# Kernel tuning notes

Measured on AMD Instinct MI355X. Metric: run time of the kernel, lower is better.

Reference implementation:

```python
import jax, jax.numpy as jnp
import numpy as np

B, S, E, H, WIN = 1, 2048, 1024, 16, 256
D = E // H  # head_out = 64


def setup_inputs() -> dict:
    key = jax.random.key(0)
    ks = jax.random.split(key, 10)
    w = lambda k: jax.random.normal(k, (E, E), jnp.float32) * 0.02
    return {
        'x': jax.random.normal(ks[0], (B, S, E), jnp.float32),
        'global_attention_mask': jax.random.randint(ks[1], (B, S), 0, 2).astype(jnp.int32),
        'W_local_query': w(ks[2]),
        'W_local_key': w(ks[3]),
        'W_local_value': w(ks[4]),
        'W_query': w(ks[5]),
        'W_key': w(ks[6]),
        'W_value': w(ks[7]),
        'W_proj': w(ks[8]),
        'b_proj': jnp.zeros((E,), jnp.float32),
    }


def reference(x, global_attention_mask, W_local_query, W_local_key, W_local_value,
              W_query, W_key, W_value, W_proj, b_proj):
    b, seq, emb = x.shape
    nH, dh, win = H, D, WIN
    chunks = seq // win
    NEG = -1e9
    scale = 1.0 / (dh ** 0.5)

    # ---- local (windowed) branch ----
    ql = x @ W_local_query            # [b,S,E]
    kl = x @ W_local_key
    vl = x @ W_local_value
    # NOTE: original does a direct .view -> plain reshape (no head transpose)
    qc = ql.reshape(b, nH, chunks, win, dh)
    kc = kl.reshape(b, nH, chunks, win, dh)
    vloc = vl.reshape(b, nH, seq, dh)
    s = jnp.einsum('bhcqd,bhckd->bhcqk', qc, kc)      # [b,H,C,W,W]
    causal_w = jnp.tril(jnp.ones((win, win), bool))
    s = jnp.where(causal_w, s, NEG) * scale           # mask then /sqrt(d), as in source
    s = s.mean(axis=2)                                # mean over chunks -> [b,H,W,W]
    s = jnp.pad(s, ((0, 0), (0, 0), (0, seq - win), (0, seq - win)))
    aw_l = jax.nn.softmax(s, axis=-1)                 # [b,H,S,S]
    local_ctx = jnp.einsum('bhqk,bhkd->bqhd', aw_l, vloc).reshape(b, seq, emb)

    # ---- global (full) branch ----
    q = (x @ W_query).reshape(b, seq, nH, dh).transpose(0, 2, 1, 3)
    k = (x @ W_key).reshape(b, seq, nH, dh).transpose(0, 2, 1, 3)
    v = (x @ W_value).reshape(b, seq, nH, dh).transpose(0, 2, 1, 3)
    sg = jnp.einsum('bhqd,bhkd->bhqk', q, k)          # [b,H,S,S]
    causal_s = jnp.tril(jnp.ones((seq, seq), bool))
    sg = jnp.where(causal_s, sg, NEG) * scale
    aw_g = jax.nn.softmax(sg, axis=-1)
    gctx = jnp.einsum('bhqk,bhkd->bqhd', aw_g, v).reshape(b, seq, emb)

    # ---- combine via global mask, then output projection ----
    ctx = jnp.where(global_attention_mask[:, :, None] == 1, gctx, local_ctx)
    return ctx @ W_proj + b_proj
```

## Files before the change

### kernel.cpp

```cpp
#include <hip/hip_runtime.h>
#include <hip/hip_bf16.h>

typedef _Float16 h8 __attribute__((ext_vector_type(8)));
typedef _Float16 h4 __attribute__((ext_vector_type(4)));
typedef _Float16 h2 __attribute__((ext_vector_type(2)));
typedef __fp16 fp16x2 __attribute__((ext_vector_type(2)));
typedef float f4 __attribute__((ext_vector_type(4)));

#define S_LEN 2048
#define EMB 1024
#define NH 16
#define DH 64

__device__ __forceinline__ void async_copy16(const void* g, void* l) {
  __builtin_amdgcn_global_load_lds(
      (const __attribute__((address_space(1))) void*)g,
      (__attribute__((address_space(3))) void*)l, 16, 0, 0);
}

__device__ __forceinline__ f4 mfma16(h8 a, h8 b, f4 c) {
  return __builtin_amdgcn_mfma_f32_16x16x32_f16(a, b, c, 0, 0, 0);
}

__device__ __forceinline__ h2 cvt_pk(float a, float b) {
  const fp16x2 r = __builtin_amdgcn_cvt_pkrtz(a, b);
  return __builtin_bit_cast(h2, r);
}

__global__ __launch_bounds__(256) void prep_kernel(
    const float* __restrict__ x, const float* w0, const float* w1, const float* w2,
    const float* w3, const float* w4, const float* w5, const float* w6,
    _Float16* __restrict__ xh, _Float16* __restrict__ Wtb,
    const int* __restrict__ gmask, int* __restrict__ qsel, int* __restrict__ qcnt) {
  const int bid = blockIdx.x;
  if (bid < 2048) {
    const int i = bid * 256 + threadIdx.x;
    const float4 v = *(const float4*)&x[(long)i * 4];
    h4 o;
    o.x = (_Float16)v.x; o.y = (_Float16)v.y; o.z = (_Float16)v.z; o.w = (_Float16)v.w;
    *(h4*)&xh[(long)i * 4] = o;
    return;
  }
  if (bid < 9216) {
    const int b2 = bid - 2048;
    const int z = b2 >> 10, rem = b2 & 1023;
    const float* W = w0;
    switch (z) {
      case 1: W = w1; break; case 2: W = w2; break; case 3: W = w3; break;
      case 4: W = w4; break; case 5: W = w5; break; case 6: W = w6; break;
      default: break;
    }
    __shared__ float t[32][33];
    const int bk = (rem & 31) * 32, bn = (rem >> 5) * 32;
    const int tx = threadIdx.x & 31, ty = threadIdx.x >> 5;
    #pragma unroll
    for (int i = 0; i < 4; ++i)
      t[ty + i * 8][tx] = W[(long)(bk + ty + i * 8) * 1024 + bn + tx];
    __syncthreads();
    _Float16* o = Wtb + (long)z * 1048576;
    #pragma unroll
    for (int i = 0; i < 4; ++i)
      o[(long)(bn + ty + i * 8) * 1024 + bk + tx] = (_Float16)t[tx][ty + i * 8];
    return;
  }
  const int t = threadIdx.x;
  int m8[8], cnt8 = 0;
  #pragma unroll
  for (int j = 0; j < 8; ++j) {
    m8[j] = gmask[t * 8 + j];
    cnt8 += (m8[j] == 1);
  }
  __shared__ int sc[256];
  sc[t] = cnt8;
  __syncthreads();
  for (int off = 1; off < 256; off <<= 1) {
    const int v = (t >= off) ? sc[t - off] : 0;
    __syncthreads();
    sc[t] += v;
    __syncthreads();
  }
  int base = sc[t] - cnt8;
  #pragma unroll
  for (int j = 0; j < 8; ++j)
    if (m8[j] == 1) qsel[base++] = t * 8 + j;
  if (t == 255) qcnt[0] = sc[255];
}

__global__ __launch_bounds__(512, 2) void gemm256_kernel(
    const _Float16* __restrict__ A, const _Float16* __restrict__ Bt,
    _Float16* __restrict__ Aq, _Float16* __restrict__ Ak,
    _Float16* __restrict__ proj234, _Float16* __restrict__ vgT) {
  const int bid = blockIdx.x;
  const int bxx = (bid >> 3) & 7;
  const int byy = (bid & 7) * 3 + (bid >> 6);
  const int bm = bxx * 256, bn = byy * 256;

  __shared__ alignas(16) _Float16 As[2][2][8192];
  __shared__ alignas(16) _Float16 Bs[2][2][8192];

  const int tid = threadIdx.x;
  const int w = tid >> 6, l = tid & 63;
  const int lo = l & 15, hi = l >> 4;
  const int wm = w >> 2, wn = w & 3;
  const int srow = tid >> 3;
  const int kseg = (tid & 7) ^ (srow & 7);

  const _Float16* Bb = Bt + (long)(byy >> 2) * 1048576 + (long)(bn & 1023) * 1024;

#define STG_A(db, half, tt) do {                                                     \
    const int t_ = (tt) < 15 ? (tt) : 15;                                            \
    const _Float16* s_ = A + (long)(bm + (half) * 128 + srow) * 1024 + t_ * 64 + kseg * 8; \
    async_copy16(s_, &As[db][half][w * 512]);                                        \
    async_copy16(s_ + 65536, &As[db][half][4096 + w * 512]);                         \
  } while (0)
#define STG_B(db, half, tt) do {                                                     \
    const int t_ = (tt) < 15 ? (tt) : 15;                                            \
    const _Float16* s_ = Bb + (long)((half) * 128 + srow) * 1024 + t_ * 64 + kseg * 8; \
    async_copy16(s_, &Bs[db][half][w * 512]);                                        \
    async_copy16(s_ + 65536, &Bs[db][half][4096 + w * 512]);                         \
  } while (0)
#define LDA(db, mg) do { _Pragma("unroll")                                           \
    for (int fr = 0; fr < 4; ++fr) {                                                 \
      const int rr = wm * 64 + fr * 16 + lo;                                         \
      _Pragma("unroll") for (int kk = 0; kk < 2; ++kk)                               \
        af[fr][kk] = *(const h8*)&As[db][mg][rr * 64 + (((kk * 4 + hi) ^ (rr & 7)) * 8)]; \
    } } while (0)
#define LDB(db, ng) do { _Pragma("unroll")                                           \
    for (int fc = 0; fc < 2; ++fc) {                                                 \
      const int rr = wn * 32 + fc * 16 + lo;                                         \
      _Pragma("unroll") for (int kk = 0; kk < 2; ++kk)                               \
        bf[ng][fc][kk] = *(const h8*)&Bs[db][ng][rr * 64 + (((kk * 4 + hi) ^ (rr & 7)) * 8)]; \
    } } while (0)
#define MFMA_PH(mg, ng) do {                                                         \
    __builtin_amdgcn_s_setprio(1);                                                   \
    _Pragma("unroll") for (int fr = 0; fr < 4; ++fr)                                 \
      _Pragma("unroll") for (int fc = 0; fc < 2; ++fc) {                             \
        acc[mg][fr][ng][fc] = mfma16(af[fr][0], bf[ng][fc][0], acc[mg][fr][ng][fc]); \
        acc[mg][fr][ng][fc] = mfma16(af[fr][1], bf[ng][fc][1], acc[mg][fr][ng][fc]); \
      }                                                                              \
    __builtin_amdgcn_s_setprio(0);                                                   \
  } while (0)
#define BARR do { asm volatile("" ::: "memory"); __builtin_amdgcn_s_barrier();       \
                  asm volatile("" ::: "memory"); } while (0)
#define VM8 asm volatile("s_waitcnt vmcnt(8)" ::: "memory")

  const f4 zero = {0.f, 0.f, 0.f, 0.f};
  f4 acc[2][4][2][2];
  #pragma unroll
  for (int a_ = 0; a_ < 2; ++a_)
    #pragma unroll
    for (int b_ = 0; b_ < 4; ++b_)
      #pragma unroll
      for (int c_ = 0; c_ < 2; ++c_)
        #pragma unroll
        for (int d_ = 0; d_ < 2; ++d_) acc[a_][b_][c_][d_] = zero;
  h8 af[4][2];
  h8 bf[2][2][2];

  STG_A(0, 0, 0); STG_B(0, 0, 0); STG_A(0, 1, 0); STG_B(0, 1, 0);
  STG_A(1, 0, 1); STG_B(1, 0, 1); STG_A(1, 1, 1);
  asm volatile("s_waitcnt vmcnt(4)" ::: "memory");
  BARR;

  for (int i = 0; i < 8; ++i) {
    const int t2 = 2 * i + 2, t3 = 2 * i + 3;
    LDA(0, 0); LDB(0, 0); STG_B(1, 1, 2 * i + 1); MFMA_PH(0, 0); VM8; BARR;
    LDB(0, 1); STG_A(0, 0, t2); MFMA_PH(0, 1); BARR;
    LDA(0, 1); STG_B(0, 0, t2); MFMA_PH(1, 0); BARR;
    STG_A(0, 1, t2); MFMA_PH(1, 1); VM8; BARR;
    LDA(1, 0); LDB(1, 0); STG_B(0, 1, t2); MFMA_PH(0, 0); VM8; BARR;
    LDB(1, 1); STG_A(1, 0, t3); MFMA_PH(0, 1); BARR;
    LDA(1, 1); STG_B(1, 0, t3); MFMA_PH(1, 0); BARR;
    STG_A(1, 1, t3); MFMA_PH(1, 1); VM8; BARR;
  }

  const int slabv = byy >> 2;
  #pragma unroll
  for (int mg = 0; mg < 2; ++mg)
    #pragma unroll
    for (int fr = 0; fr < 4; ++fr) {
      const int row0 = bm + mg * 128 + wm * 64 + fr * 16 + hi * 4;
      #pragma unroll
      for (int ng = 0; ng < 2; ++ng)
        #pragma unroll
        for (int fc = 0; fc < 2; ++fc) {
          const int colg = bn + ng * 128 + wn * 32 + fc * 16 + lo;
          const int e = colg & 1023;
          if (slabv <= 1) {
            _Float16* dst = (slabv == 0) ? Aq : Ak;
            #pragma unroll
            for (int r = 0; r < 4; ++r) {
              const int s = row0 + r;
              const long off = (long)(((s >> 7) * 256 + (s & 15) * 16 + (e >> 6))) * 512
                               + ((s >> 4) & 7) * 64 + (e & 63);
              dst[off] = (_Float16)acc[mg][fr][ng][fc][r];
            }
          } else if (slabv == 5) {
            const h2 a = cvt_pk(acc[mg][fr][ng][fc][0], acc[mg][fr][ng][fc][1]);
            const h2 b = cvt_pk(acc[mg][fr][ng][fc][2], acc[mg][fr][ng][fc][3]);
            const h4 v4 = {a[0], a[1], b[0], b[1]};
            *(h4*)&vgT[(long)e * 2048 + row0] = v4;
          } else {
            _Float16* cp = proj234 + (long)(slabv - 2) * 2097152 + (long)row0 * 1024 + e;
            #pragma unroll
            for (int r = 0; r < 4; ++r)
              cp[(long)r * 1024] = (_Float16)acc[mg][fr][ng][fc][r];
          }
        }
    }
#undef STG_A
#undef STG_B
#undef LDA
#undef LDB
#undef MFMA_PH
#undef BARR
#undef VM8
}

__global__ __launch_bounds__(256) void flash_kernel(
    const _Float16* __restrict__ Q, const _Float16* __restrict__ Km,
    const _Float16* __restrict__ Vt, const int* __restrict__ qsel,
    const int* __restrict__ qcnt, _Float16* __restrict__ ctx,
    _Float16* __restrict__ pO, float2* __restrict__ ml,
    const _Float16* __restrict__ Aq, const _Float16* __restrict__ Ak,
    _Float16* __restrict__ P, const _Float16* __restrict__ vl,
    float* __restrict__ Vall, float* __restrict__ Vtail) {
  __shared__ alignas(16) char smem[43008];
  const int bx = blockIdx.x;
  const int tid = threadIdx.x;

  if (bx >= 1280) {
    const int hh = bx - 1280;
    const int d = tid & 63, g = tid >> 6;
    float sall = 0.f, shead = 0.f;
    for (int i = 0; i < 32; ++i) {
      const int ro = g * 32 + i;
      const _Float16* base = vl + (long)(hh * 128 + ro) * 1024 + d;
      #pragma unroll
      for (int j = 0; j < 16; ++j) {
        const float v = (float)base[j * 64];
        sall += v;
        if (ro < 16) shead += v;
      }
    }
    float* sA = (float*)smem;
    float* sH = (float*)(smem + 1024);
    sA[g * 64 + d] = sall; sH[g * 64 + d] = shead;
    __syncthreads();
    if (g == 0) {
      const float a = sA[d] + sA[64 + d] + sA[128 + d] + sA[192 + d];
      const float hsum = sH[d] + sH[64 + d] + sH[128 + d] + sH[192 + d];
      Vall[hh * 64 + d] = a;
      Vtail[hh * 64 + d] = a - hsum;
    }
    return;
  }

  if (bx >= 1024) {
    const int b = bx - 1024;
    const int hh = b >> 4, sub = b & 15;
    const int bm = (sub >> 2) * 64, bn = (sub & 3) * 64;
    const _Float16* Ab = Aq + (long)hh * 131072;
    const _Float16* Bb = Ak + (long)hh * 131072;
    _Float16* As = (_Float16*)smem;
    _Float16* Bs = (_Float16*)(smem + 8192);
    const int w = tid >> 6, l = tid & 63;
    const int lo = l & 15, hi = l >> 4;
    const int srow = tid >> 3;
    const int ssl = (tid & 7) ^ (srow & 7);

    const f4 zero = {0.f, 0.f, 0.f, 0.f};
    f4 acc[4];
    #pragma unroll
    for (int n = 0; n < 4; ++n) acc[n] = zero;

    for (int k0 = 0; k0 < 512; k0 += 64) {
      async_copy16(&Ab[(long)(bm + srow) * 512 + k0 + ssl * 8], &As[(w * 8) * 64]);
      async_copy16(&Ab[(long)(bm + 32 + srow) * 512 + k0 + ssl * 8], &As[(w * 8 + 32) * 64]);
      async_copy16(&Bb[(long)(bn + srow) * 512 + k0 + ssl * 8], &Bs[(w * 8) * 64]);
      async_copy16(&Bb[(long)(bn + 32 + srow) * 512 + k0 + ssl * 8], &Bs[(w * 8 + 32) * 64]);
      __syncthreads();
      #pragma unroll
      for (int kk = 0; kk < 2; ++kk) {
        const int ra = w * 16 + lo;
        const h8 af = *(const h8*)&As[ra * 64 + (((kk * 4 + hi) ^ (ra & 7)) * 8)];
        #pragma unroll
        for (int n = 0; n < 4; ++n) {
          const int rb = n * 16 + lo;
          const h8 bff = *(const h8*)&Bs[rb * 64 + (((kk * 4 + hi) ^ (rb & 7)) * 8)];
          acc[n] = mfma16(af, bff, acc[n]);
        }
      }
      __syncthreads();
    }
    #pragma unroll
    for (int n = 0; n < 4; ++n) {
      const int col = bn + n * 16 + lo;
      const int row0 = bm + w * 16 + hi * 4;
      #pragma unroll
      for (int r = 0; r < 4; ++r)
        P[(long)hh * 65536 + (long)(row0 + r) * 256 + col] = (_Float16)acc[n][r];
    }
    return;
  }

  const int h = bx & 15;
  const int v = bx >> 4;
  const int tile = 31 - (v >> 1);
  const int chunk = v & 1;
  int cnt = qcnt[0];
  cnt = cnt < 1 ? 1 : (cnt > 2048 ? 2048 : cnt);
  if (tile * 64 >= cnt) return;
  const int L = (qsel[min(tile * 64 + 63, cnt - 1)] & 2047) + 1;
  const int ntot = (L + 63) >> 6;
  const bool chunked = (ntot > 16);
  if (!chunked && chunk) return;
  const int nsplit = chunked ? ((ntot + 1) >> 1) : ntot;
  const int t0 = chunk ? nsplit : 0;
  const int t1 = chunk ? ntot : nsplit;

  const int w = tid >> 6, l = tid & 63;
  const int lo = l & 15, hi = l >> 4;
  const int row = tile * 64 + w * 16 + lo;
  const int qg = qsel[min(row, cnt - 1)] & 2047;

  _Float16* KsB = (_Float16*)smem;
  _Float16* VsB = (_Float16*)(smem + 16384);
  _Float16* ps = (_Float16*)(smem + 32768) + w * 1280;

  const int rl = tid >> 3;
  const int ssl = (tid & 7) ^ (rl & 7);

#define STAGE(b, t)                                                                   \
  do {                                                                                \
    async_copy16(&Km[(long)((t) * 64 + rl) * EMB + h * DH + ssl * 8],                 \
                 &KsB[(b) * 4096 + (w * 8) * 64]);                                    \
    async_copy16(&Km[(long)((t) * 64 + 32 + rl) * EMB + h * DH + ssl * 8],            \
                 &KsB[(b) * 4096 + (w * 8 + 32) * 64]);                               \
    async_copy16(&Vt[(long)(h * DH + rl) * S_LEN + (t) * 64 + ssl * 8],               \
                 &VsB[(b) * 4096 + (w * 8) * 64]);                                    \
    async_copy16(&Vt[(long)(h * DH + 32 + rl) * S_LEN + (t) * 64 + ssl * 8],          \
                 &VsB[(b) * 4096 + (w * 8 + 32) * 64]);                               \
  } while (0)

  h8 qf[2];
  #pragma unroll
  for (int kk = 0; kk < 2; ++kk)
    qf[kk] = *(const h8*)&Q[(long)qg * EMB + h * DH + kk * 32 + hi * 8];

  const f4 zero = {0.f, 0.f, 0.f, 0.f};
  f4 o[4];
  #pragma unroll
  for (int nd = 0; nd < 4; ++nd) o[nd] = zero;
  float mr = -1e30f, lr = 0.f;
  const float SC = 0.125f * 1.44269504f;

  STAGE(0, t0);
  __syncthreads();
  int cur = 0;

  for (int t = t0; t < t1; ++t) {
    if (t + 1 < t1) STAGE(cur ^ 1, t + 1);

    const _Float16* ks = KsB + cur * 4096;
    const _Float16* vs = VsB + cur * 4096;

    __builtin_amdgcn_s_setprio(1);
    f4 s[4];
    #pragma unroll
    for (int n = 0; n < 4; ++n) {
      s[n] = zero;
      #pragma unroll
      for (int kk = 0; kk < 2; ++kk) {
        const int r = n * 16 + lo;
        const h8 kf = *(const h8*)&ks[r * 64 + (((kk * 4 + hi) ^ (lo & 7)) * 8)];
        s[n] = mfma16(kf, qf[kk], s[n]);
      }
    }
    __builtin_amdgcn_s_setprio(0);

    float sv[16];
    float tm = -1e30f;
    #pragma unroll
    for (int n = 0; n < 4; ++n)
      #pragma unroll
      for (int r = 0; r < 4; ++r) {
        float vv = s[n][r] * SC;
        if ((t * 64 + n * 16 + hi * 4 + r) > qg) vv = -1e30f;
        sv[n * 4 + r] = vv;
        tm = fmaxf(tm, vv);
      }
    tm = fmaxf(tm, __shfl_xor(tm, 16));
    tm = fmaxf(tm, __shfl_xor(tm, 32));
    const float mn = fmaxf(mr, tm);
    const float c = exp2f(mr - mn);
    mr = mn;
    float psum = 0.f;
    #pragma unroll
    for (int i = 0; i < 16; ++i) {
      sv[i] = exp2f(sv[i] - mr);
      psum += sv[i];
    }
    psum += __shfl_xor(psum, 16);
    psum += __shfl_xor(psum, 32);
    lr = lr * c + psum;

    #pragma unroll
    for (int n = 0; n < 4; ++n) {
      const int seg = (2 * n + (hi >> 1)) ^ (lo & 7);
      const int base = lo * 80 + seg * 8 + (hi & 1) * 4;
      *(h2*)&ps[base] = cvt_pk(sv[n * 4 + 0], sv[n * 4 + 1]);
      *(h2*)&ps[base + 2] = cvt_pk(sv[n * 4 + 2], sv[n * 4 + 3]);
    }
    h8 pb[2];
    #pragma unroll
    for (int kk = 0; kk < 2; ++kk)
      pb[kk] = *(const h8*)&ps[lo * 80 + (((kk * 4 + hi) ^ (lo & 7)) * 8)];

    __builtin_amdgcn_s_setprio(1);
    #pragma unroll
    for (int nd = 0; nd < 4; ++nd) {
      #pragma unroll
      for (int r = 0; r < 4; ++r) o[nd][r] *= c;
      #pragma unroll
      for (int kk = 0; kk < 2; ++kk) {
        const int rr = nd * 16 + lo;
        const h8 vf = *(const h8*)&vs[rr * 64 + (((kk * 4 + hi) ^ (lo & 7)) * 8)];
        o[nd] = mfma16(vf, pb[kk], o[nd]);
      }
    }
    __builtin_amdgcn_s_setprio(0);

    __syncthreads();
    cur ^= 1;
  }
#undef STAGE

  if (chunked) {
    const int slot = (h * 32 + tile) * 2 + chunk;
    _Float16* po = pO + (long)slot * 4096 + (w * 16 + lo) * 64;
    #pragma unroll
    for (int nd = 0; nd < 4; ++nd) {
      const h2 a = cvt_pk(o[nd][0], o[nd][1]);
      const h2 b = cvt_pk(o[nd][2], o[nd][3]);
      const h4 v4 = {a[0], a[1], b[0], b[1]};
      *(h4*)&po[nd * 16 + hi * 4] = v4;
    }
    if (hi == 0) ml[slot * 64 + w * 16 + lo] = make_float2(mr, lr);
  } else if (row < cnt) {
    const float inv = 1.f / lr;
    #pragma unroll
    for (int nd = 0; nd < 4; ++nd) {
      const h2 a = cvt_pk(o[nd][0] * inv, o[nd][1] * inv);
      const h2 b = cvt_pk(o[nd][2] * inv, o[nd][3] * inv);
      const h4 v4 = {a[0], a[1], b[0], b[1]};
      *(h4*)&ctx[(long)qg * EMB + h * DH + nd * 16 + hi * 4] = v4;
    }
  }
}

__global__ __launch_bounds__(256) void localfin_kernel(
    const _Float16* __restrict__ P, const _Float16* __restrict__ vl,
    const float* __restrict__ Vall, const float* __restrict__ Vtail,
    const _Float16* __restrict__ pO, const float2* __restrict__ ml,
    const int* __restrict__ gmask, const int* __restrict__ qsel,
    const int* __restrict__ qcnt, _Float16* __restrict__ ctx) {
  const int bid = blockIdx.x;
  const int tid = threadIdx.x;
  if (bid < 1024) {
    const int q = bid & 255, hg = bid >> 8;
    if (gmask[q] == 1) return;
    const int sub = tid >> 6, l = tid & 63;
    const int hh = hg * 4 + sub;
    __shared__ float wgt[4][256];
    const _Float16* Pr = P + ((long)hh * 256 + q) * 256;
    float sv[4];
    bool valid[4];
    float M = -1e30f;
    #pragma unroll
    for (int i = 0; i < 4; ++i) {
      const int k = l + i * 64;
      valid[i] = (k <= q);
      sv[i] = valid[i] ? (float)Pr[k] * 0.015625f : -1e30f;
      M = fmaxf(M, sv[i]);
    }
    M = fmaxf(M, __shfl_xor(M, 1));
    M = fmaxf(M, __shfl_xor(M, 2));
    M = fmaxf(M, __shfl_xor(M, 4));
    M = fmaxf(M, __shfl_xor(M, 8));
    M = fmaxf(M, __shfl_xor(M, 16));
    M = fmaxf(M, __shfl_xor(M, 32));
    M = fmaxf(M, 0.f);
    float ps = 0.f;
    #pragma unroll
    for (int i = 0; i < 4; ++i) {
      const float e = valid[i] ? __expf(sv[i] - M) : 0.f;
      wgt[sub][l + i * 64] = e;
      ps += e;
    }
    ps += __shfl_xor(ps, 1);
    ps += __shfl_xor(ps, 2);
    ps += __shfl_xor(ps, 4);
    ps += __shfl_xor(ps, 8);
    ps += __shfl_xor(ps, 16);
    ps += __shfl_xor(ps, 32);
    const float em = __expf(-M);
    const float denom = ps + 1792.f * em;
    const int d = l;
    float acc = em * Vtail[hh * 64 + d];
    const _Float16* vb = vl + (long)hh * 128 * 1024 + d;
    for (int k = 0; k <= q; ++k)
      acc += wgt[sub][k] * (float)vb[(long)(k >> 4) * 1024 + (k & 15) * 64];
    ctx[(long)q * EMB + hh * DH + d] = (_Float16)(acc / denom);
    return;
  }
  if (bid < 1536) {
    const int b2 = bid - 1024;
    const int h = b2 & 15, tile = b2 >> 4;
    int cnt = qcnt[0];
    cnt = cnt < 1 ? 1 : (cnt > 2048 ? 2048 : cnt);
    if (tile * 64 >= cnt) return;
    const int L = (qsel[min(tile * 64 + 63, cnt - 1)] & 2047) + 1;
    if (((L + 63) >> 6) <= 16) return;
    const int q = tid >> 2, ds = (tid & 3) * 16;
    const int row = tile * 64 + q;
    if (row >= cnt) return;
    const int sg = qsel[row] & 2047;
    const int slot0 = (h * 32 + tile) * 2, slot1 = slot0 + 1;
    const float2 ml0 = ml[slot0 * 64 + q];
    const float2 ml1 = ml[slot1 * 64 + q];
    const float M = fmaxf(ml0.x, ml1.x);
    const float w0 = exp2f(ml0.x - M), w1 = exp2f(ml1.x - M);
    const float inv = 1.f / (w0 * ml0.y + w1 * ml1.y);
    const h8 a0 = *(const h8*)&pO[(long)slot0 * 4096 + q * 64 + ds];
    const h8 a1 = *(const h8*)&pO[(long)slot0 * 4096 + q * 64 + ds + 8];
    const h8 b0 = *(const h8*)&pO[(long)slot1 * 4096 + q * 64 + ds];
    const h8 b1 = *(const h8*)&pO[(long)slot1 * 4096 + q * 64 + ds + 8];
    h8 r0, r1;
    #pragma unroll
    for (int j = 0; j < 8; ++j) {
      r0[j] = (_Float16)((w0 * (float)a0[j] + w1 * (float)b0[j]) * inv);
      r1[j] = (_Float16)((w0 * (float)a1[j] + w1 * (float)b1[j]) * inv);
    }
    *(h8*)&ctx[(long)sg * EMB + h * DH + ds] = r0;
    *(h8*)&ctx[(long)sg * EMB + h * DH + ds + 8] = r1;
    return;
  }
  const int gid = (bid - 1536) * 256 + tid;
  const int s = 256 + (gid >> 7), e8 = (gid & 127) * 8;
  if (gmask[s] == 0) {
    h8 v;
    #pragma unroll
    for (int j = 0; j < 8; ++j)
      v[j] = (_Float16)(Vall[e8 + j] * (1.f / 2048.f));
    *(h8*)&ctx[(long)s * EMB + e8] = v;
  }
}

__global__ __launch_bounds__(256) void gemm64_kernel(
    const _Float16* __restrict__ A, const _Float16* __restrict__ Bt,
    float* __restrict__ C, const float* __restrict__ bias) {
  const int bm = blockIdx.x * 64, bn = blockIdx.y * 64;
  __shared__ alignas(16) _Float16 As[2][4096];
  __shared__ alignas(16) _Float16 Bs[2][4096];
  const int tid = threadIdx.x;
  const int w = tid >> 6, l = tid & 63;
  const int lo = l & 15, hi = l >> 4;
  const int srow = tid >> 3;
  const int ssl = (tid & 7) ^ (srow & 7);

#define STG64(b, k0) do {                                                            \
    async_copy16(&A[(long)(bm + srow) * 1024 + (k0) + ssl * 8], &As[b][(w * 8) * 64]); \
    async_copy16(&A[(long)(bm + 32 + srow) * 1024 + (k0) + ssl * 8],                 \
                 &As[b][(w * 8 + 32) * 64]);                                         \
    async_copy16(&Bt[(long)(bn + srow) * 1024 + (k0) + ssl * 8], &Bs[b][(w * 8) * 64]); \
    async_copy16(&Bt[(long)(bn + 32 + srow) * 1024 + (k0) + ssl * 8],                \
                 &Bs[b][(w * 8 + 32) * 64]);                                         \
  } while (0)

  const f4 zero = {0.f, 0.f, 0.f, 0.f};
  f4 acc[4];
  #pragma unroll
  for (int n = 0; n < 4; ++n) acc[n] = zero;

  STG64(0, 0);
  __syncthreads();
  int cur = 0;
  for (int k0 = 0; k0 < 1024; k0 += 64) {
    if (k0 + 64 < 1024) STG64(cur ^ 1, k0 + 64);
    #pragma unroll
    for (int kk = 0; kk < 2; ++kk) {
      const int ra = w * 16 + lo;
      const h8 af = *(const h8*)&As[cur][ra * 64 + (((kk * 4 + hi) ^ (ra & 7)) * 8)];
      #pragma unroll
      for (int n = 0; n < 4; ++n) {
        const int rb = n * 16 + lo;
        const h8 bff = *(const h8*)&Bs[cur][rb * 64 + (((kk * 4 + hi) ^ (rb & 7)) * 8)];
        acc[n] = mfma16(af, bff, acc[n]);
      }
    }
    __syncthreads();
    cur ^= 1;
  }
#undef STG64

  #pragma unroll
  for (int n = 0; n < 4; ++n) {
    const int col = bn + n * 16 + lo;
    const float bv = bias[col];
    const int row0 = bm + w * 16 + hi * 4;
    #pragma unroll
    for (int r = 0; r < 4; ++r)
      C[(long)(row0 + r) * 1024 + col] = acc[n][r] + bv;
  }
}

extern "C" void kernel_launch(void* const* d_in, const int* in_sizes, int n_in,
                              void* d_out, int out_size, void* d_ws, size_t ws_size,
                              hipStream_t stream) {
  const float* x = (const float*)d_in[0];
  const int* gmask = (const int*)d_in[1];
  const float* Wlq = (const float*)d_in[2];
  const float* Wlk = (const float*)d_in[3];
  const float* Wlv = (const float*)d_in[4];
  const float* Wq = (const float*)d_in[5];
  const float* Wk = (const float*)d_in[6];
  const float* Wv = (const float*)d_in[7];
  const float* Wp = (const float*)d_in[8];
  const float* bp = (const float*)d_in[9];
  float* out = (float*)d_out;

  char* ws = (char*)d_ws;
  _Float16* xh = (_Float16*)(ws);
  _Float16* Wtb = (_Float16*)(ws + (4u << 20));
  _Float16* pO = (_Float16*)(ws);
  _Float16* ctx = (_Float16*)(ws + (8u << 20));
  _Float16* P = (_Float16*)(ws + (12u << 20));
  float* Vall = (float*)(ws + (14u << 20));
  float* Vtail = (float*)(ws + (14u << 20) + 4096);
  float2* ml = (float2*)(ws + (14u << 20) + 16384);
  _Float16* Wpt = (_Float16*)(ws + (16u << 20));
  _Float16* Aq = (_Float16*)(ws + (18u << 20));
  _Float16* Ak = (_Float16*)(ws + (22u << 20));
  _Float16* proj234 = (_Float16*)(ws + (26u << 20));
  _Float16* vl = proj234;
  _Float16* qg = (_Float16*)(ws + (30u << 20));
  _Float16* kg = (_Float16*)(ws + (34u << 20));
  _Float16* vgT = (_Float16*)(ws + (38u << 20));
  int* qsel = (int*)(ws + (42u << 20));
  int* qcnt = (int*)(ws + (42u << 20) + 8192);

  prep_kernel<<<9217, 256, 0, stream>>>(x, Wlq, Wlk, Wlv, Wq, Wk, Wv, Wp, xh, Wtb,
                                        gmask, qsel, qcnt);
  gemm256_kernel<<<192, 512, 0, stream>>>(xh, Wtb, Aq, Ak, proj234, vgT);
  flash_kernel<<<1296, 256, 0, stream>>>(qg, kg, vgT, qsel, qcnt, ctx, pO, ml,
                                         Aq, Ak, P, vl, Vall, Vtail);
  localfin_kernel<<<2432, 256, 0, stream>>>(P, vl, Vall, Vtail, pO, ml, gmask,
                                            qsel, qcnt, ctx);
  gemm64_kernel<<<dim3(32, 16), 256, 0, stream>>>(ctx, Wpt, out, bp);
}
```

Baseline: 115.8 us.

## Split local-attention finalize per head and reorder flash kernel block dispatch

The local finalize branch now uses one block per (query, head) and splits the sequential k loop across four waves, combining their partial sums through shared memory. Previously each wave walked up to 256 keys serially for one head. The flash kernel also moves the small local-score GEMM and V-sum blocks to the lowest block indices so they are scheduled first, ahead of the long flash tiles. This adds block-level syncs and quadruples the finalize grid.

```diff
diff --git a/kernel.cpp b/kernel.cpp
--- a/kernel.cpp
+++ b/kernel.cpp
@@ -229,36 +229,8 @@
   const int bx = blockIdx.x;
   const int tid = threadIdx.x;
 
-  if (bx >= 1280) {
-    const int hh = bx - 1280;
-    const int d = tid & 63, g = tid >> 6;
-    float sall = 0.f, shead = 0.f;
-    for (int i = 0; i < 32; ++i) {
-      const int ro = g * 32 + i;
-      const _Float16* base = vl + (long)(hh * 128 + ro) * 1024 + d;
-      #pragma unroll
-      for (int j = 0; j < 16; ++j) {
-        const float v = (float)base[j * 64];
-        sall += v;
-        if (ro < 16) shead += v;
-      }
-    }
-    float* sA = (float*)smem;
-    float* sH = (float*)(smem + 1024);
-    sA[g * 64 + d] = sall; sH[g * 64 + d] = shead;
-    __syncthreads();
-    if (g == 0) {
-      const float a = sA[d] + sA[64 + d] + sA[128 + d] + sA[192 + d];
-      const float hsum = sH[d] + sH[64 + d] + sH[128 + d] + sH[192 + d];
-      Vall[hh * 64 + d] = a;
-      Vtail[hh * 64 + d] = a - hsum;
-    }
-    return;
-  }
-
-  if (bx >= 1024) {
-    const int b = bx - 1024;
-    const int hh = b >> 4, sub = b & 15;
+  if (bx < 256) {
+    const int hh = bx >> 4, sub = bx & 15;
     const int bm = (sub >> 2) * 64, bn = (sub & 3) * 64;
     const _Float16* Ab = Aq + (long)hh * 131072;
     const _Float16* Bb = Ak + (long)hh * 131072;
@@ -304,8 +276,36 @@
     return;
   }
 
-  const int h = bx & 15;
-  const int v = bx >> 4;
+  if (bx < 272) {
+    const int hh = bx - 256;
+    const int d = tid & 63, g = tid >> 6;
+    float sall = 0.f, shead = 0.f;
+    for (int i = 0; i < 32; ++i) {
+      const int ro = g * 32 + i;
+      const _Float16* base = vl + (long)(hh * 128 + ro) * 1024 + d;
+      #pragma unroll
+      for (int j = 0; j < 16; ++j) {
+        const float v = (float)base[j * 64];
+        sall += v;
+        if (ro < 16) shead += v;
+      }
+    }
+    float* sA = (float*)smem;
+    float* sH = (float*)(smem + 1024);
+    sA[g * 64 + d] = sall; sH[g * 64 + d] = shead;
+    __syncthreads();
+    if (g == 0) {
+      const float a = sA[d] + sA[64 + d] + sA[128 + d] + sA[192 + d];
+      const float hsum = sH[d] + sH[64 + d] + sH[128 + d] + sH[192 + d];
+      Vall[hh * 64 + d] = a;
+      Vtail[hh * 64 + d] = a - hsum;
+    }
+    return;
+  }
+
+  const int fx = bx - 272;
+  const int h = fx & 15;
+  const int v = fx >> 4;
   const int tile = 31 - (v >> 1);
   const int chunk = v & 1;
   int cnt = qcnt[0];
@@ -467,55 +467,61 @@
     const int* __restrict__ qcnt, _Float16* __restrict__ ctx) {
   const int bid = blockIdx.x;
   const int tid = threadIdx.x;
-  if (bid < 1024) {
-    const int q = bid & 255, hg = bid >> 8;
+  if (bid < 4096) {
+    const int q = bid & 255, hh = bid >> 8;
     if (gmask[q] == 1) return;
-    const int sub = tid >> 6, l = tid & 63;
-    const int hh = hg * 4 + sub;
-    __shared__ float wgt[4][256];
+    const int l = tid & 63, g = tid >> 6;
+    __shared__ float wgt[256];
+    __shared__ float red[4];
+    __shared__ float pacc[4][64];
     const _Float16* Pr = P + ((long)hh * 256 + q) * 256;
-    float sv[4];
-    bool valid[4];
-    float M = -1e30f;
-    #pragma unroll
-    for (int i = 0; i < 4; ++i) {
-      const int k = l + i * 64;
-      valid[i] = (k <= q);
-      sv[i] = valid[i] ? (float)Pr[k] * 0.015625f : -1e30f;
-      M = fmaxf(M, sv[i]);
-    }
+    const int k = tid;
+    const bool valid = (k <= q);
+    const float sv = valid ? (float)Pr[k] * 0.015625f : -1e30f;
+    float M = sv;
     M = fmaxf(M, __shfl_xor(M, 1));
     M = fmaxf(M, __shfl_xor(M, 2));
     M = fmaxf(M, __shfl_xor(M, 4));
     M = fmaxf(M, __shfl_xor(M, 8));
     M = fmaxf(M, __shfl_xor(M, 16));
     M = fmaxf(M, __shfl_xor(M, 32));
+    if (l == 0) red[g] = M;
+    __syncthreads();
+    M = fmaxf(fmaxf(red[0], red[1]), fmaxf(red[2], red[3]));
     M = fmaxf(M, 0.f);
-    float ps = 0.f;
-    #pragma unroll
-    for (int i = 0; i < 4; ++i) {
-      const float e = valid[i] ? __expf(sv[i] - M) : 0.f;
-      wgt[sub][l + i * 64] = e;
-      ps += e;
-    }
+    const float e = valid ? __expf(sv - M) : 0.f;
+    wgt[k] = e;
+    float ps = e;
     ps += __shfl_xor(ps, 1);
     ps += __shfl_xor(ps, 2);
     ps += __shfl_xor(ps, 4);
     ps += __shfl_xor(ps, 8);
     ps += __shfl_xor(ps, 16);
     ps += __shfl_xor(ps, 32);
+    __syncthreads();
+    if (l == 0) red[g] = ps;
+    __syncthreads();
     const float em = __expf(-M);
-    const float denom = ps + 1792.f * em;
-    const int d = l;
-    float acc = em * Vtail[hh * 64 + d];
-    const _Float16* vb = vl + (long)hh * 128 * 1024 + d;
-    for (int k = 0; k <= q; ++k)
-      acc += wgt[sub][k] * (float)vb[(long)(k >> 4) * 1024 + (k & 15) * 64];
-    ctx[(long)q * EMB + hh * DH + d] = (_Float16)(acc / denom);
+    const float denom = red[0] + red[1] + red[2] + red[3] + 1792.f * em;
+    float acc = 0.f;
+    const _Float16* vb = vl + (long)hh * 128 * 1024 + l;
+    const int kbeg = g * 64;
+    for (int j = 0; j < 64; ++j) {
+      const int kk = kbeg + j;
+      if (kk > q) break;
+      acc += wgt[kk] * (float)vb[(long)(kk >> 4) * 1024 + (kk & 15) * 64];
+    }
+    pacc[g][l] = acc;
+    __syncthreads();
+    if (g == 0) {
+      const float a = pacc[0][l] + pacc[1][l] + pacc[2][l] + pacc[3][l]
+                      + em * Vtail[hh * 64 + l];
+      ctx[(long)q * EMB + hh * DH + l] = (_Float16)(a / denom);
+    }
     return;
   }
-  if (bid < 1536) {
-    const int b2 = bid - 1024;
+  if (bid < 4608) {
+    const int b2 = bid - 4096;
     const int h = b2 & 15, tile = b2 >> 4;
     int cnt = qcnt[0];
     cnt = cnt < 1 ? 1 : (cnt > 2048 ? 2048 : cnt);
@@ -546,7 +552,7 @@
     *(h8*)&ctx[(long)sg * EMB + h * DH + ds + 8] = r1;
     return;
   }
-  const int gid = (bid - 1536) * 256 + tid;
+  const int gid = (bid - 4608) * 256 + tid;
   const int s = 256 + (gid >> 7), e8 = (gid & 127) * 8;
   if (gmask[s] == 0) {
     h8 v;
@@ -655,7 +661,7 @@
   gemm256_kernel<<<192, 512, 0, stream>>>(xh, Wtb, Aq, Ak, proj234, vgT);
   flash_kernel<<<1296, 256, 0, stream>>>(qg, kg, vgT, qsel, qcnt, ctx, pO, ml,
                                          Aq, Ak, P, vl, Vall, Vtail);
-  localfin_kernel<<<2432, 256, 0, stream>>>(P, vl, Vall, Vtail, pO, ml, gmask,
+  localfin_kernel<<<5504, 256, 0, stream>>>(P, vl, Vall, Vtail, pO, ml, gmask,
                                             qsel, qcnt, ctx);
   gemm64_kernel<<<dim3(32, 16), 256, 0, stream>>>(ctx, Wpt, out, bp);
 }
```

New measurement: 144.0 us. 24.3% more time.
